# Kernel optimization log

Measured on AMD Instinct MI355X. Metric: run time of the kernel, lower is better.

## Reference

```python
import jax, jax.numpy as jnp
import numpy as np

B, N, DIM, H, DH = 8, 1024, 768, 12, 64
INNER = H * DH
SCALE = DH ** -0.5


def _bias_idx(n):
    # Reproduce the offset->id mapping from the torch __init__ loop:
    # offsets are first seen in row-major (p1, p2) order, so
    # id(0)=0, id(-k)=k (k=1..n-1), id(+k)=n-1+k.
    i = np.arange(n)[:, None]
    j = np.arange(n)[None, :]
    off = i - j
    idx = np.where(off <= 0, -off, n - 1 + off)
    return jnp.asarray(idx, dtype=jnp.int32)  # (n, n), values in [0, 2n-2]


def setup_inputs() -> dict:
    key = jax.random.key(0)
    ks = jax.random.split(key, 5)
    x = jax.random.normal(ks[0], (B, N, DIM), dtype=jnp.float32)
    w_qkv = jax.random.normal(ks[1], (DIM, 3 * INNER), dtype=jnp.float32) * (DIM ** -0.5)
    bias_table = jax.random.normal(ks[2], (H, 2 * N - 1), dtype=jnp.float32) * 0.02
    w_out = jax.random.normal(ks[3], (INNER, DIM), dtype=jnp.float32) * (INNER ** -0.5)
    b_out = jnp.zeros((DIM,), dtype=jnp.float32)
    bias_idx = _bias_idx(N)
    return {"x": x, "w_qkv": w_qkv, "bias_table": bias_table,
            "w_out": w_out, "b_out": b_out, "bias_idx": bias_idx}


def reference(x, w_qkv, bias_table, w_out, b_out, bias_idx):
    b, n, _ = x.shape
    qkv = x @ w_qkv  # (b, n, 3*inner)
    q, k, v = jnp.split(qkv, 3, axis=-1)
    def heads(t):
        return t.reshape(b, n, H, DH).transpose(0, 2, 1, 3)  # (b, h, n, d)
    q, k, v = heads(q), heads(k), heads(v)
    bias = bias_table[:, bias_idx]  # (h, n, n), gathered per-head relpos bias
    dots = jnp.einsum('bhid,bhjd->bhij', q, k) * SCALE + bias[None]
    attn = jax.nn.softmax(dots, axis=-1)
    out = jnp.einsum('bhij,bhjd->bhid', attn, v)
    out = out.transpose(0, 2, 1, 3).reshape(b, n, INNER)
    return out @ w_out + b_out
```

## Files before the change

### kernel.cpp

```cpp
#include <hip/hip_runtime.h>
#include <hip/hip_bf16.h>
#include <stdint.h>

typedef unsigned short u16;
typedef unsigned int u32;
typedef __bf16 bf16x8 __attribute__((ext_vector_type(8)));
typedef _Float16 f16x8 __attribute__((ext_vector_type(8)));
typedef float f32x4 __attribute__((ext_vector_type(4)));
typedef float f32x16 __attribute__((ext_vector_type(16)));
typedef unsigned short u16x4 __attribute__((ext_vector_type(4)));
typedef unsigned int u32x4 __attribute__((ext_vector_type(4)));

#define SEQ     1024
#define DIM     768
#define NH      12
#define QKV_LD  2304
#define LOG2E   1.4426950408889634f
#define C1      0.18033688f

__device__ __forceinline__ float bf2f(u16 u) {
    union { unsigned v; float f; } x; x.v = ((unsigned)u) << 16; return x.f;
}
__device__ __forceinline__ u16 f2bf(float f) {
    union { float f; unsigned v; } x; x.f = f;
    unsigned r = (x.v + 0x7FFFu + ((x.v >> 16) & 1u)) >> 16;
    return (u16)r;
}
__device__ __forceinline__ void store_out(u16* p, float v)  { *p = f2bf(v); }
__device__ __forceinline__ void store_out(float* p, float v){ *p = v; }

__device__ __forceinline__ void async16(void* lds, const void* g) {
    __builtin_amdgcn_global_load_lds(
        (const __attribute__((address_space(1))) unsigned*)(uintptr_t)g,
        (__attribute__((address_space(3))) unsigned*)(unsigned)(uintptr_t)lds,
        16, 0, 0);
}

__global__ __launch_bounds__(256) void cvt_k(const float* __restrict__ in,
                                             u16* __restrict__ out) {
    int i = (blockIdx.x * 256 + threadIdx.x) * 4;
    float4 v = *(const float4*)(in + i);
    u16x4 o = { f2bf(v.x), f2bf(v.y), f2bf(v.z), f2bf(v.w) };
    *(u16x4*)(out + i) = o;
}

__global__ __launch_bounds__(256) void transpose_k(const float* __restrict__ in,
                                                   u16* __restrict__ out,
                                                   int R, int C) {
    __shared__ __align__(16) float t[32][33];
    int c0 = blockIdx.x * 32, r0 = blockIdx.y * 32;
    int tx = threadIdx.x & 31, ty = threadIdx.x >> 5;
#pragma unroll
    for (int i = 0; i < 32; i += 8)
        t[ty + i][tx] = in[(size_t)(r0 + ty + i) * C + c0 + tx];
    __syncthreads();
#pragma unroll
    for (int i = 0; i < 32; i += 8)
        out[(size_t)(c0 + ty + i) * R + r0 + tx] = f2bf(t[tx][ty + i]);
}

__global__ __launch_bounds__(256) void vt_k(const u16* __restrict__ qkv,
                                            _Float16* __restrict__ vT) {
    __shared__ __align__(16) u16 t[32][33];
    int bh = blockIdx.z;
    int b = bh / 12, h = bh % 12;
    int key0 = blockIdx.x * 32, dh0 = blockIdx.y * 32;
    int tx = threadIdx.x & 31, ty = threadIdx.x >> 5;
#pragma unroll
    for (int i = 0; i < 32; i += 8)
        t[ty + i][tx] = qkv[(size_t)(b * SEQ + key0 + ty + i) * QKV_LD +
                            1536 + h * 64 + dh0 + tx];
    __syncthreads();
#pragma unroll
    for (int i = 0; i < 32; i += 8)
        vT[(size_t)(bh * 64 + dh0 + ty + i) * SEQ + key0 + tx] =
            (_Float16)bf2f(t[tx][ty + i]);
}

template <int HAS_BIAS, typename OUT_T>
__global__ __launch_bounds__(256) void gemm_bt(const u16* __restrict__ A,
                                               const u16* __restrict__ Bt,
                                               const float* __restrict__ bias,
                                               OUT_T* __restrict__ C,
                                               int M, int N, int K) {
    __shared__ __align__(16) u16 sA[128 * 64];
    __shared__ __align__(16) u16 sB[128 * 64];
    const int tid = threadIdx.x;
    const int lane = tid & 63;
    const int quad = lane >> 4, l16 = lane & 15;
    const int wave = tid >> 6;
    const int m0 = blockIdx.x * 128, n0 = blockIdx.y * 128;
    const int wm = (wave >> 1) * 64, wn = (wave & 1) * 64;

    const int co0 = (quad ^ (l16 & 7)) * 8;
    f32x4 acc[4][4] = {};

    for (int k0 = 0; k0 < K; k0 += 64) {
        __syncthreads();
#pragma unroll
        for (int rep = 0; rep < 4; ++rep) {
            int i = rep * 256 + tid;
            int row = i >> 3;
            int c = (i & 7) ^ (row & 7);
            async16(&sA[i * 8], A + (size_t)(m0 + row) * K + k0 + c * 8);
            async16(&sB[i * 8], Bt + (size_t)(n0 + row) * K + k0 + c * 8);
        }
        __syncthreads();

#pragma unroll
        for (int ks = 0; ks < 2; ++ks) {
            const int co = co0 ^ (ks * 32);
            bf16x8 af[4], bfr[4];
#pragma unroll
            for (int mi = 0; mi < 4; ++mi)
                af[mi] = *(const bf16x8*)&sA[(wm + mi * 16 + l16) * 64 + co];
#pragma unroll
            for (int nj = 0; nj < 4; ++nj)
                bfr[nj] = *(const bf16x8*)&sB[(wn + nj * 16 + l16) * 64 + co];
#pragma unroll
            for (int mi = 0; mi < 4; ++mi)
#pragma unroll
                for (int nj = 0; nj < 4; ++nj)
                    acc[mi][nj] = __builtin_amdgcn_mfma_f32_16x16x32_bf16(
                        af[mi], bfr[nj], acc[mi][nj], 0, 0, 0);
        }
    }

#pragma unroll
    for (int mi = 0; mi < 4; ++mi) {
#pragma unroll
        for (int nj = 0; nj < 4; ++nj) {
            int col = n0 + wn + nj * 16 + l16;
            float bv = HAS_BIAS ? bias[col] : 0.0f;
#pragma unroll
            for (int r = 0; r < 4; ++r) {
                int row = m0 + wm + mi * 16 + quad * 4 + r;
                store_out(&C[(size_t)row * N + col], acc[mi][nj][r] + bv);
            }
        }
    }
}

__global__ __launch_bounds__(256, 3) void attn_k(const u16* __restrict__ qkv,
                                                 const _Float16* __restrict__ vT,
                                                 const float* __restrict__ bias_table,
                                                 u16* __restrict__ out) {
    __shared__ __align__(16) u16 sK[2][64 * 64];
    __shared__ __align__(16) _Float16 sV[2][64 * 64];
    __shared__ __align__(16) float sLut[2048];

    const int tid = threadIdx.x;
    const int wave = tid >> 6, lane = tid & 63;
    const int l31 = lane & 31, hi = lane >> 5;
    const int bh = blockIdx.x;
    const int b = bh / NH, h = bh % NH;
    const int q0 = blockIdx.y * 128, wq = wave * 32;

    for (int i = tid; i < 2047; i += 256)
        sLut[i] = LOG2E * bias_table[h * 2047 + (i <= 1023 ? 1023 - i : i)];

    bf16x8 qf[4];
#pragma unroll
    for (int ks = 0; ks < 4; ++ks)
        qf[ks] = *(const bf16x8*)(qkv +
            (size_t)(b * SEQ + q0 + wq + l31) * QKV_LD + h * 64 + ks * 16 + hi * 8);

    const u16* kgp[2];
    const _Float16* vgp[2];
    int lds_i[2];
#pragma unroll
    for (int rep = 0; rep < 2; ++rep) {
        int i = rep * 256 + wave * 64 + lane;
        int row = i >> 3;
        int c = (i & 7) ^ (row & 7);
        kgp[rep] = qkv + (size_t)(b * SEQ + row) * QKV_LD + 768 + h * 64 + c * 8;
        vgp[rep] = vT + (size_t)(bh * 64 + row) * SEQ + c * 8;
        lds_i[rep] = i * 8;
    }

    const int ib0 = 1023 + q0 + wq + l31;
    const int hi4 = hi * 4;

#pragma unroll
    for (int rep = 0; rep < 2; ++rep) {
        async16(&sK[0][lds_i[rep]], kgp[rep]);
        async16(&sV[0][lds_i[rep]], vgp[rep]);
        kgp[rep] += (size_t)64 * QKV_LD;
        vgp[rep] += 64;
    }
    __syncthreads();

    f32x16 o[2] = {};
    f32x16 osum = {};
    const u32x4 onebits = { 0x3C003C00u, 0x3C003C00u, 0x3C003C00u, 0x3C003C00u };
    const f16x8 ones = __builtin_bit_cast(f16x8, onebits);

    for (int kt = 0; kt < SEQ / 64; ++kt) {
        const int cur = kt & 1;
        if (kt + 1 < SEQ / 64) {
            const int nxt = cur ^ 1;
#pragma unroll
            for (int rep = 0; rep < 2; ++rep) {
                async16(&sK[nxt][lds_i[rep]], kgp[rep]);
                async16(&sV[nxt][lds_i[rep]], vgp[rep]);
                kgp[rep] += (size_t)64 * QKV_LD;
                vgp[rep] += 64;
            }
        }
        const u16* sKc = sK[cur];
        const _Float16* sVc = sV[cur];

        f16x8 pfrag[4];
#pragma unroll
        for (int t = 0; t < 2; ++t) {
            const u16* kr = sKc + (t * 32 + l31) * 64;
            f32x16 s = {};
#pragma unroll
            for (int ks = 0; ks < 4; ++ks) {
                int slot = (2 * ks + hi) ^ (l31 & 7);
                bf16x8 af = *(const bf16x8*)(kr + slot * 8);
                s = __builtin_amdgcn_mfma_f32_32x32x16_bf16(af, qf[ks], s, 0, 0, 0);
            }
            const int ibt = ib0 - kt * 64 - t * 32 - hi4;
            u32 wlo[4], whi[4];
#pragma unroll
            for (int g = 0; g < 4; ++g) {
                const float* bw = &sLut[ibt - 8 * g];
                float p0 = __builtin_amdgcn_exp2f(s[4 * g + 0] * C1 + bw[0]);
                float p1 = __builtin_amdgcn_exp2f(s[4 * g + 1] * C1 + bw[-1]);
                float p2 = __builtin_amdgcn_exp2f(s[4 * g + 2] * C1 + bw[-2]);
                float p3 = __builtin_amdgcn_exp2f(s[4 * g + 3] * C1 + bw[-3]);
                wlo[g] = __builtin_bit_cast(u32, __builtin_amdgcn_cvt_pkrtz(p0, p1));
                whi[g] = __builtin_bit_cast(u32, __builtin_amdgcn_cvt_pkrtz(p2, p3));
            }
#pragma unroll
            for (int c = 0; c < 2; ++c) {
                auto rlo = __builtin_amdgcn_permlane32_swap(
                    wlo[2 * c], wlo[2 * c + 1], false, false);
                auto rhi = __builtin_amdgcn_permlane32_swap(
                    whi[2 * c], whi[2 * c + 1], false, false);
                u32x4 f = { rlo[0], rhi[0], rlo[1], rhi[1] };
                pfrag[t * 2 + c] = __builtin_bit_cast(f16x8, f);
            }
        }

#pragma unroll
        for (int kg = 0; kg < 4; ++kg)
            osum = __builtin_amdgcn_mfma_f32_32x32x16_f16(ones, pfrag[kg], osum, 0, 0, 0);
#pragma unroll
        for (int dt = 0; dt < 2; ++dt) {
            const _Float16* vr = sVc + (dt * 32 + l31) * 64;
#pragma unroll
            for (int kg = 0; kg < 4; ++kg) {
                int slot = (2 * kg + hi) ^ (l31 & 7);
                f16x8 vf = *(const f16x8*)(vr + slot * 8);
                o[dt] = __builtin_amdgcn_mfma_f32_32x32x16_f16(vf, pfrag[kg], o[dt], 0, 0, 0);
            }
        }
        __syncthreads();
    }

    float inv = __builtin_amdgcn_rcpf(osum[0]);
    size_t rowbase = (size_t)(b * SEQ + q0 + wq + l31) * DIM + h * 64 + hi4;
#pragma unroll
    for (int dt = 0; dt < 2; ++dt) {
#pragma unroll
        for (int g = 0; g < 4; ++g) {
            u16x4 pk = { f2bf(o[dt][4 * g + 0] * inv), f2bf(o[dt][4 * g + 1] * inv),
                         f2bf(o[dt][4 * g + 2] * inv), f2bf(o[dt][4 * g + 3] * inv) };
            *(u16x4*)&out[rowbase + dt * 32 + 8 * g] = pk;
        }
    }
}

extern "C" void kernel_launch(void* const* d_in, const int* in_sizes, int n_in,
                              void* d_out, int out_size, void* d_ws, size_t ws_size,
                              hipStream_t stream) {
    const float* x          = (const float*)d_in[0];
    const float* w_qkv      = (const float*)d_in[1];
    const float* bias_table = (const float*)d_in[2];
    const float* w_out      = (const float*)d_in[3];
    const float* b_out      = (const float*)d_in[4];
    float* out = (float*)d_out;

    char* ws = (char*)d_ws;
    u16* ws_qkv        = (u16*)(ws);
    u16* ws_attn       = (u16*)(ws + 37748736);
    u16* ws_xb         = (u16*)(ws + 50331648);
    u16* ws_wqkvT      = (u16*)(ws + 62914560);
    u16* ws_woutT      = (u16*)(ws + 66453504);
    _Float16* ws_vT    = (_Float16*)(ws + 67633152);

    cvt_k<<<8 * 1024 * 768 / 1024, 256, 0, stream>>>(x, ws_xb);
    transpose_k<<<dim3(2304 / 32, 768 / 32), 256, 0, stream>>>(w_qkv, ws_wqkvT, 768, 2304);
    transpose_k<<<dim3(768 / 32, 768 / 32), 256, 0, stream>>>(w_out, ws_woutT, 768, 768);

    gemm_bt<0, u16><<<dim3(8192 / 128, 2304 / 128), 256, 0, stream>>>(
        ws_xb, ws_wqkvT, nullptr, ws_qkv, 8192, 2304, 768);

    vt_k<<<dim3(SEQ / 32, 2, 8 * NH), 256, 0, stream>>>(ws_qkv, ws_vT);

    attn_k<<<dim3(8 * NH, SEQ / 128, 1), 256, 0, stream>>>(ws_qkv, ws_vT, bias_table, ws_attn);

    gemm_bt<1, float><<<dim3(8192 / 128, 768 / 128), 256, 0, stream>>>(
        ws_attn, ws_woutT, b_out, out, 8192, 768, 768);
}
```

Measured before the change: 198.6 us.

## Software-pipeline attention loop so PV of previous tile overlaps QK and exp

Restructures the flash-attention inner loop so the P·V and row-sum MFMAs for tile kt-1 are issued alongside the QK^T MFMAs for tile kt. The V fragments are held in registers across iterations, and the exp/pack of the current scores runs after those matrix ops. The intent is to let exp/VALU work overlap MFMA latency rather than serialize behind it. s_setprio raises wave priority around the MFMA block. The cost is more live registers (vf[8], pf, sAcc), which could reduce occupancy or cause spills.

```diff
diff --git a/kernel.cpp b/kernel.cpp
--- a/kernel.cpp
+++ b/kernel.cpp
@@ -180,6 +180,7 @@
 
     const int ib0 = 1023 + q0 + wq + l31;
     const int hi4 = hi * 4;
+    const int l7 = l31 & 7;
 
 #pragma unroll
     for (int rep = 0; rep < 2; ++rep) {
@@ -195,70 +196,112 @@
     const u32x4 onebits = { 0x3C003C00u, 0x3C003C00u, 0x3C003C00u, 0x3C003C00u };
     const f16x8 ones = __builtin_bit_cast(f16x8, onebits);
 
-    for (int kt = 0; kt < SEQ / 64; ++kt) {
+    f16x8 pf[4];
+    f16x8 vf[8];
+
+#define QK_TILE(sKc, kt, sAcc)                                                 \
+    _Pragma("unroll")                                                          \
+    for (int t = 0; t < 2; ++t) {                                              \
+        const u16* kr = (sKc) + (t * 32 + l31) * 64;                           \
+        f32x16 s = {};                                                         \
+        _Pragma("unroll")                                                      \
+        for (int ks = 0; ks < 4; ++ks) {                                       \
+            int slot = (2 * ks + hi) ^ l7;                                     \
+            bf16x8 af = *(const bf16x8*)(kr + slot * 8);                       \
+            s = __builtin_amdgcn_mfma_f32_32x32x16_bf16(af, qf[ks], s, 0, 0, 0); \
+        }                                                                      \
+        sAcc[t] = s;                                                           \
+    }
+
+#define PV_PREV()                                                              \
+    _Pragma("unroll")                                                          \
+    for (int kg = 0; kg < 4; ++kg)                                             \
+        osum = __builtin_amdgcn_mfma_f32_32x32x16_f16(ones, pf[kg], osum, 0, 0, 0); \
+    _Pragma("unroll")                                                          \
+    for (int dt = 0; dt < 2; ++dt)                                             \
+        _Pragma("unroll")                                                      \
+        for (int kg = 0; kg < 4; ++kg)                                         \
+            o[dt] = __builtin_amdgcn_mfma_f32_32x32x16_f16(                    \
+                vf[dt * 4 + kg], pf[kg], o[dt], 0, 0, 0);
+
+#define LOAD_V(sVc)                                                            \
+    _Pragma("unroll")                                                          \
+    for (int dt = 0; dt < 2; ++dt) {                                           \
+        const _Float16* vr = (sVc) + (dt * 32 + l31) * 64;                     \
+        _Pragma("unroll")                                                      \
+        for (int kg = 0; kg < 4; ++kg) {                                       \
+            int slot = (2 * kg + hi) ^ l7;                                     \
+            vf[dt * 4 + kg] = *(const f16x8*)(vr + slot * 8);                  \
+        }                                                                      \
+    }
+
+#define EXP_PACK(kt, sAcc)                                                     \
+    _Pragma("unroll")                                                          \
+    for (int t = 0; t < 2; ++t) {                                              \
+        const int ibt = ib0 - (kt) * 64 - t * 32 - hi4;                        \
+        u32 wlo[4], whi[4];                                                    \
+        _Pragma("unroll")                                                      \
+        for (int g = 0; g < 4; ++g) {                                          \
+            const float* bw = &sLut[ibt - 8 * g];                              \
+            float p0 = __builtin_amdgcn_exp2f(sAcc[t][4 * g + 0] * C1 + bw[0]);  \
+            float p1 = __builtin_amdgcn_exp2f(sAcc[t][4 * g + 1] * C1 + bw[-1]); \
+            float p2 = __builtin_amdgcn_exp2f(sAcc[t][4 * g + 2] * C1 + bw[-2]); \
+            float p3 = __builtin_amdgcn_exp2f(sAcc[t][4 * g + 3] * C1 + bw[-3]); \
+            wlo[g] = __builtin_bit_cast(u32, __builtin_amdgcn_cvt_pkrtz(p0, p1)); \
+            whi[g] = __builtin_bit_cast(u32, __builtin_amdgcn_cvt_pkrtz(p2, p3)); \
+        }                                                                      \
+        _Pragma("unroll")                                                      \
+        for (int c = 0; c < 2; ++c) {                                          \
+            auto rlo = __builtin_amdgcn_permlane32_swap(                       \
+                wlo[2 * c], wlo[2 * c + 1], false, false);                     \
+            auto rhi = __builtin_amdgcn_permlane32_swap(                       \
+                whi[2 * c], whi[2 * c + 1], false, false);                     \
+            u32x4 fw = { rlo[0], rhi[0], rlo[1], rhi[1] };                     \
+            pf[t * 2 + c] = __builtin_bit_cast(f16x8, fw);                     \
+        }                                                                      \
+    }
+
+#define PREFETCH(nxt)                                                          \
+    _Pragma("unroll")                                                          \
+    for (int rep = 0; rep < 2; ++rep) {                                        \
+        async16(&sK[nxt][lds_i[rep]], kgp[rep]);                               \
+        async16(&sV[nxt][lds_i[rep]], vgp[rep]);                               \
+        kgp[rep] += (size_t)64 * QKV_LD;                                       \
+        vgp[rep] += 64;                                                        \
+    }
+
+    {
+        PREFETCH(1)
+        f32x16 sAcc[2];
+        QK_TILE(sK[0], 0, sAcc)
+        LOAD_V(sV[0])
+        EXP_PACK(0, sAcc)
+        __syncthreads();
+    }
+
+    for (int kt = 1; kt < SEQ / 64; ++kt) {
         const int cur = kt & 1;
-        if (kt + 1 < SEQ / 64) {
-            const int nxt = cur ^ 1;
-#pragma unroll
-            for (int rep = 0; rep < 2; ++rep) {
-                async16(&sK[nxt][lds_i[rep]], kgp[rep]);
-                async16(&sV[nxt][lds_i[rep]], vgp[rep]);
-                kgp[rep] += (size_t)64 * QKV_LD;
-                vgp[rep] += 64;
-            }
-        }
+        if (kt + 1 < SEQ / 64) { PREFETCH(cur ^ 1) }
         const u16* sKc = sK[cur];
         const _Float16* sVc = sV[cur];
 
-        f16x8 pfrag[4];
-#pragma unroll
-        for (int t = 0; t < 2; ++t) {
-            const u16* kr = sKc + (t * 32 + l31) * 64;
-            f32x16 s = {};
-#pragma unroll
-            for (int ks = 0; ks < 4; ++ks) {
-                int slot = (2 * ks + hi) ^ (l31 & 7);
-                bf16x8 af = *(const bf16x8*)(kr + slot * 8);
-                s = __builtin_amdgcn_mfma_f32_32x32x16_bf16(af, qf[ks], s, 0, 0, 0);
-            }
-            const int ibt = ib0 - kt * 64 - t * 32 - hi4;
-            u32 wlo[4], whi[4];
-#pragma unroll
-            for (int g = 0; g < 4; ++g) {
-                const float* bw = &sLut[ibt - 8 * g];
-                float p0 = __builtin_amdgcn_exp2f(s[4 * g + 0] * C1 + bw[0]);
-                float p1 = __builtin_amdgcn_exp2f(s[4 * g + 1] * C1 + bw[-1]);
-                float p2 = __builtin_amdgcn_exp2f(s[4 * g + 2] * C1 + bw[-2]);
-                float p3 = __builtin_amdgcn_exp2f(s[4 * g + 3] * C1 + bw[-3]);
-                wlo[g] = __builtin_bit_cast(u32, __builtin_amdgcn_cvt_pkrtz(p0, p1));
-                whi[g] = __builtin_bit_cast(u32, __builtin_amdgcn_cvt_pkrtz(p2, p3));
-            }
-#pragma unroll
-            for (int c = 0; c < 2; ++c) {
-                auto rlo = __builtin_amdgcn_permlane32_swap(
-                    wlo[2 * c], wlo[2 * c + 1], false, false);
-                auto rhi = __builtin_amdgcn_permlane32_swap(
-                    whi[2 * c], whi[2 * c + 1], false, false);
-                u32x4 f = { rlo[0], rhi[0], rlo[1], rhi[1] };
-                pfrag[t * 2 + c] = __builtin_bit_cast(f16x8, f);
-            }
-        }
-
-#pragma unroll
-        for (int kg = 0; kg < 4; ++kg)
-            osum = __builtin_amdgcn_mfma_f32_32x32x16_f16(ones, pfrag[kg], osum, 0, 0, 0);
-#pragma unroll
-        for (int dt = 0; dt < 2; ++dt) {
-            const _Float16* vr = sVc + (dt * 32 + l31) * 64;
-#pragma unroll
-            for (int kg = 0; kg < 4; ++kg) {
-                int slot = (2 * kg + hi) ^ (l31 & 7);
-                f16x8 vf = *(const f16x8*)(vr + slot * 8);
-                o[dt] = __builtin_amdgcn_mfma_f32_32x32x16_f16(vf, pfrag[kg], o[dt], 0, 0, 0);
-            }
-        }
-        __syncthreads();
-    }
+        f32x16 sAcc[2];
+        __builtin_amdgcn_s_setprio(1);
+        QK_TILE(sKc, kt, sAcc)
+        PV_PREV()
+        __builtin_amdgcn_s_setprio(0);
+        LOAD_V(sVc)
+        EXP_PACK(kt, sAcc)
+        if (kt + 1 < SEQ / 64) __syncthreads();
+    }
+
+    PV_PREV()
+
+#undef QK_TILE
+#undef PV_PREV
+#undef LOAD_V
+#undef EXP_PACK
+#undef PREFETCH
 
     float inv = __builtin_amdgcn_rcpf(osum[0]);
     size_t rowbase = (size_t)(b * SEQ + q0 + wq + l31) * DIM + h * 64 + hi4;
```

Result: no change. 198.4 us (-0.1%).

## Load V fragments directly from global and use fp16 shifted bias LUTs

Applied to the files above, without the earlier changes.

The attention kernel no longer stages V tiles through shared memory. Each wave reads its V fragments straight from global memory into registers at the start of each key tile. The fp32 bias LUT is replaced by four pre-shifted fp16 copies, so each lane can fetch four consecutive bias values with one aligned vector load instead of four scalar loads. QK MFMAs are also grouped before the softmax, and the PV MFMAs run under raised wave priority. This cuts LDS usage, which may allow more occupancy, but it exposes global-load latency on V and adds fp16 rounding to the bias.

```diff
diff --git a/kernel.cpp b/kernel.cpp
--- a/kernel.cpp
+++ b/kernel.cpp
@@ -6,6 +6,7 @@
 typedef unsigned int u32;
 typedef __bf16 bf16x8 __attribute__((ext_vector_type(8)));
 typedef _Float16 f16x8 __attribute__((ext_vector_type(8)));
+typedef _Float16 f16x4 __attribute__((ext_vector_type(4)));
 typedef float f32x4 __attribute__((ext_vector_type(4)));
 typedef float f32x16 __attribute__((ext_vector_type(16)));
 typedef unsigned short u16x4 __attribute__((ext_vector_type(4)));
@@ -146,8 +147,7 @@
                                                  const float* __restrict__ bias_table,
                                                  u16* __restrict__ out) {
     __shared__ __align__(16) u16 sK[2][64 * 64];
-    __shared__ __align__(16) _Float16 sV[2][64 * 64];
-    __shared__ __align__(16) float sLut[2048];
+    __shared__ __align__(16) _Float16 sLutH[4 * 2052];
 
     const int tid = threadIdx.x;
     const int wave = tid >> 6, lane = tid & 63;
@@ -156,8 +156,15 @@
     const int b = bh / NH, h = bh % NH;
     const int q0 = blockIdx.y * 128, wq = wave * 32;
 
-    for (int i = tid; i < 2047; i += 256)
-        sLut[i] = LOG2E * bias_table[h * 2047 + (i <= 1023 ? 1023 - i : i)];
+#pragma unroll
+    for (int j = 0; j < 4; ++j)
+        for (int u = tid; u < 2052; u += 256) {
+            int z = 2047 - u - j;
+            float v = 0.f;
+            if (z >= 0 && z <= 2046)
+                v = LOG2E * bias_table[h * 2047 + (z <= 1023 ? 1023 - z : z)];
+            sLutH[j * 2052 + u] = (_Float16)v;
+        }
 
     bf16x8 qf[4];
 #pragma unroll
@@ -166,7 +173,6 @@
             (size_t)(b * SEQ + q0 + wq + l31) * QKV_LD + h * 64 + ks * 16 + hi * 8);
 
     const u16* kgp[2];
-    const _Float16* vgp[2];
     int lds_i[2];
 #pragma unroll
     for (int rep = 0; rep < 2; ++rep) {
@@ -174,19 +180,21 @@
         int row = i >> 3;
         int c = (i & 7) ^ (row & 7);
         kgp[rep] = qkv + (size_t)(b * SEQ + row) * QKV_LD + 768 + h * 64 + c * 8;
-        vgp[rep] = vT + (size_t)(bh * 64 + row) * SEQ + c * 8;
         lds_i[rep] = i * 8;
     }
 
-    const int ib0 = 1023 + q0 + wq + l31;
+    const _Float16* vb0 = vT + (size_t)(bh * 64 + l31) * SEQ + hi * 8;
+
+    const int r0 = (-l31) & 3;
+    const _Float16* lutp = sLutH + (r0 * 2052 - r0);
+    const int ub0 = 1024 - q0 - wq - l31 + hi * 4;
+    const int l7 = l31 & 7;
     const int hi4 = hi * 4;
 
 #pragma unroll
     for (int rep = 0; rep < 2; ++rep) {
         async16(&sK[0][lds_i[rep]], kgp[rep]);
-        async16(&sV[0][lds_i[rep]], vgp[rep]);
         kgp[rep] += (size_t)64 * QKV_LD;
-        vgp[rep] += 64;
     }
     __syncthreads();
 
@@ -198,38 +206,49 @@
     for (int kt = 0; kt < SEQ / 64; ++kt) {
         const int cur = kt & 1;
         if (kt + 1 < SEQ / 64) {
-            const int nxt = cur ^ 1;
 #pragma unroll
             for (int rep = 0; rep < 2; ++rep) {
-                async16(&sK[nxt][lds_i[rep]], kgp[rep]);
-                async16(&sV[nxt][lds_i[rep]], vgp[rep]);
+                async16(&sK[cur ^ 1][lds_i[rep]], kgp[rep]);
                 kgp[rep] += (size_t)64 * QKV_LD;
-                vgp[rep] += 64;
-            }
-        }
+            }
+        }
+
+        f16x8 vf[8];
+#pragma unroll
+        for (int dt = 0; dt < 2; ++dt)
+#pragma unroll
+            for (int kg = 0; kg < 4; ++kg)
+                vf[dt * 4 + kg] =
+                    *(const f16x8*)(vb0 + (size_t)dt * 32 * SEQ + kt * 64 + kg * 16);
+
         const u16* sKc = sK[cur];
-        const _Float16* sVc = sV[cur];
-
-        f16x8 pfrag[4];
+
+        f32x16 sAcc[2];
 #pragma unroll
         for (int t = 0; t < 2; ++t) {
             const u16* kr = sKc + (t * 32 + l31) * 64;
             f32x16 s = {};
 #pragma unroll
             for (int ks = 0; ks < 4; ++ks) {
-                int slot = (2 * ks + hi) ^ (l31 & 7);
+                int slot = (2 * ks + hi) ^ l7;
                 bf16x8 af = *(const bf16x8*)(kr + slot * 8);
                 s = __builtin_amdgcn_mfma_f32_32x32x16_bf16(af, qf[ks], s, 0, 0, 0);
             }
-            const int ibt = ib0 - kt * 64 - t * 32 - hi4;
+            sAcc[t] = s;
+        }
+
+        f16x8 pf[4];
+#pragma unroll
+        for (int t = 0; t < 2; ++t) {
+            const int ub = ub0 + kt * 64 + t * 32;
             u32 wlo[4], whi[4];
 #pragma unroll
             for (int g = 0; g < 4; ++g) {
-                const float* bw = &sLut[ibt - 8 * g];
-                float p0 = __builtin_amdgcn_exp2f(s[4 * g + 0] * C1 + bw[0]);
-                float p1 = __builtin_amdgcn_exp2f(s[4 * g + 1] * C1 + bw[-1]);
-                float p2 = __builtin_amdgcn_exp2f(s[4 * g + 2] * C1 + bw[-2]);
-                float p3 = __builtin_amdgcn_exp2f(s[4 * g + 3] * C1 + bw[-3]);
+                f16x4 bw4 = *(const f16x4*)(lutp + ub + 8 * g);
+                float p0 = __builtin_amdgcn_exp2f(sAcc[t][4 * g + 0] * C1 + (float)bw4[0]);
+                float p1 = __builtin_amdgcn_exp2f(sAcc[t][4 * g + 1] * C1 + (float)bw4[1]);
+                float p2 = __builtin_amdgcn_exp2f(sAcc[t][4 * g + 2] * C1 + (float)bw4[2]);
+                float p3 = __builtin_amdgcn_exp2f(sAcc[t][4 * g + 3] * C1 + (float)bw4[3]);
                 wlo[g] = __builtin_bit_cast(u32, __builtin_amdgcn_cvt_pkrtz(p0, p1));
                 whi[g] = __builtin_bit_cast(u32, __builtin_amdgcn_cvt_pkrtz(p2, p3));
             }
@@ -239,24 +258,23 @@
                     wlo[2 * c], wlo[2 * c + 1], false, false);
                 auto rhi = __builtin_amdgcn_permlane32_swap(
                     whi[2 * c], whi[2 * c + 1], false, false);
-                u32x4 f = { rlo[0], rhi[0], rlo[1], rhi[1] };
-                pfrag[t * 2 + c] = __builtin_bit_cast(f16x8, f);
-            }
-        }
-
+                u32x4 fw = { rlo[0], rhi[0], rlo[1], rhi[1] };
+                pf[t * 2 + c] = __builtin_bit_cast(f16x8, fw);
+            }
+        }
+
+        __builtin_amdgcn_s_setprio(1);
 #pragma unroll
         for (int kg = 0; kg < 4; ++kg)
-            osum = __builtin_amdgcn_mfma_f32_32x32x16_f16(ones, pfrag[kg], osum, 0, 0, 0);
-#pragma unroll
-        for (int dt = 0; dt < 2; ++dt) {
-            const _Float16* vr = sVc + (dt * 32 + l31) * 64;
-#pragma unroll
-            for (int kg = 0; kg < 4; ++kg) {
-                int slot = (2 * kg + hi) ^ (l31 & 7);
-                f16x8 vf = *(const f16x8*)(vr + slot * 8);
-                o[dt] = __builtin_amdgcn_mfma_f32_32x32x16_f16(vf, pfrag[kg], o[dt], 0, 0, 0);
-            }
-        }
+            osum = __builtin_amdgcn_mfma_f32_32x32x16_f16(ones, pf[kg], osum, 0, 0, 0);
+#pragma unroll
+        for (int dt = 0; dt < 2; ++dt)
+#pragma unroll
+            for (int kg = 0; kg < 4; ++kg)
+                o[dt] = __builtin_amdgcn_mfma_f32_32x32x16_f16(
+                    vf[dt * 4 + kg], pf[kg], o[dt], 0, 0, 0);
+        __builtin_amdgcn_s_setprio(0);
+
         __syncthreads();
     }
 
```

New measurement: 215.6 us. 1.09x slower.

## Pre-swizzle K and V into MFMA fragment layout and drop LDS staging in attention

Applied to the files above, without the earlier changes.

Adds prep kernels that rewrite K and V per head into the exact per-lane MFMA fragment order, so the attention kernel loads operands straight from global memory into registers. This removes the LDS double buffer, async copies and per-tile barriers, and the kernel now raises wave priority around the PV MFMAs. The GEMM also remaps workgroup IDs so that each XCD works on a contiguous range of M tiles, aiming at better L2 reuse. The cost is one extra prep launch plus more global and L2 traffic per wave, since every wave reloads K and V without sharing them through LDS. ws_xb is reused as the K-fragment buffer once the QKV GEMM has finished with it.

```diff
diff --git a/kernel.cpp b/kernel.cpp
--- a/kernel.cpp
+++ b/kernel.cpp
@@ -9,6 +9,7 @@
 typedef float f32x4 __attribute__((ext_vector_type(4)));
 typedef float f32x16 __attribute__((ext_vector_type(16)));
 typedef unsigned short u16x4 __attribute__((ext_vector_type(4)));
+typedef unsigned short u16x8 __attribute__((ext_vector_type(8)));
 typedef unsigned int u32x4 __attribute__((ext_vector_type(4)));
 
 #define SEQ     1024
@@ -59,22 +60,52 @@
         out[(size_t)(c0 + ty + i) * R + r0 + tx] = f2bf(t[tx][ty + i]);
 }
 
-__global__ __launch_bounds__(256) void vt_k(const u16* __restrict__ qkv,
-                                            _Float16* __restrict__ vT) {
-    __shared__ __align__(16) u16 t[32][33];
-    int bh = blockIdx.z;
-    int b = bh / 12, h = bh % 12;
-    int key0 = blockIdx.x * 32, dh0 = blockIdx.y * 32;
-    int tx = threadIdx.x & 31, ty = threadIdx.x >> 5;
-#pragma unroll
-    for (int i = 0; i < 32; i += 8)
-        t[ty + i][tx] = qkv[(size_t)(b * SEQ + key0 + ty + i) * QKV_LD +
-                            1536 + h * 64 + dh0 + tx];
+__global__ __launch_bounds__(256) void kprep_k(const u16* __restrict__ qkv,
+                                               u16* __restrict__ kf) {
+    __shared__ u16 t2[64][68];
+    const int kt = blockIdx.x, bh = blockIdx.y;
+    const int b = bh / NH, h = bh % NH;
+    const int tid = threadIdx.x;
+    const int row = tid >> 2, c0 = (tid & 3) * 16;
+    const u16* src = qkv + (size_t)(b * SEQ + kt * 64 + row) * QKV_LD + 768 + h * 64 + c0;
+#pragma unroll
+    for (int q = 0; q < 4; ++q)
+        *(u16x4*)&t2[row][c0 + q * 4] = *(const u16x4*)(src + q * 4);
     __syncthreads();
 #pragma unroll
-    for (int i = 0; i < 32; i += 8)
-        vT[(size_t)(bh * 64 + dh0 + ty + i) * SEQ + key0 + tx] =
-            (_Float16)bf2f(t[tx][ty + i]);
+    for (int u = tid; u < 512; u += 256) {
+        int f = u >> 6, lane = u & 63;
+        int t = f >> 2, ks = f & 3;
+        int hi = lane >> 5, l31 = lane & 31;
+        const u16* p = &t2[t * 32 + l31][ks * 16 + hi * 8];
+        u16x8 w = { p[0], p[1], p[2], p[3], p[4], p[5], p[6], p[7] };
+        *(u16x8*)&kf[((((size_t)bh * 16 + kt) * 8 + f) * 64 + lane) * 8] = w;
+    }
+}
+
+__global__ __launch_bounds__(256) void vprep_k(const u16* __restrict__ qkv,
+                                               _Float16* __restrict__ vf) {
+    __shared__ u16 t2[64][68];
+    const int kt = blockIdx.x, bh = blockIdx.y;
+    const int b = bh / NH, h = bh % NH;
+    const int tid = threadIdx.x;
+    const int row = tid >> 2, c0 = (tid & 3) * 16;
+    const u16* src = qkv + (size_t)(b * SEQ + kt * 64 + row) * QKV_LD + 1536 + h * 64 + c0;
+#pragma unroll
+    for (int q = 0; q < 4; ++q)
+        *(u16x4*)&t2[row][c0 + q * 4] = *(const u16x4*)(src + q * 4);
+    __syncthreads();
+#pragma unroll
+    for (int u = tid; u < 512; u += 256) {
+        int c = u >> 6, lane = u & 63;
+        int dt = c >> 2, kg = c & 3;
+        int hi = lane >> 5, l31 = lane & 31;
+        f16x8 w;
+#pragma unroll
+        for (int j = 0; j < 8; ++j)
+            w[j] = (_Float16)bf2f(t2[kg * 16 + hi * 8 + j][dt * 32 + l31]);
+        *(f16x8*)&vf[((((size_t)bh * 16 + kt) * 8 + c) * 64 + lane) * 8] = w;
+    }
 }
 
 template <int HAS_BIAS, typename OUT_T>
@@ -89,7 +120,12 @@
     const int lane = tid & 63;
     const int quad = lane >> 4, l16 = lane & 15;
     const int wave = tid >> 6;
-    const int m0 = blockIdx.x * 128, n0 = blockIdx.y * 128;
+
+    const int wgid = blockIdx.y * gridDim.x + blockIdx.x;
+    const int xcd = wgid & 7, idx = wgid >> 3;
+    const int CM = gridDim.x >> 3;
+    const int m0 = (xcd * CM + idx % CM) * 128;
+    const int n0 = (idx / CM) * 128;
     const int wm = (wave >> 1) * 64, wn = (wave & 1) * 64;
 
     const int co0 = (quad ^ (l16 & 7)) * 8;
@@ -142,11 +178,10 @@
 }
 
 __global__ __launch_bounds__(256, 3) void attn_k(const u16* __restrict__ qkv,
-                                                 const _Float16* __restrict__ vT,
+                                                 const u16* __restrict__ kfr,
+                                                 const _Float16* __restrict__ vfr,
                                                  const float* __restrict__ bias_table,
                                                  u16* __restrict__ out) {
-    __shared__ __align__(16) u16 sK[2][64 * 64];
-    __shared__ __align__(16) _Float16 sV[2][64 * 64];
     __shared__ __align__(16) float sLut[2048];
 
     const int tid = threadIdx.x;
@@ -165,29 +200,12 @@
         qf[ks] = *(const bf16x8*)(qkv +
             (size_t)(b * SEQ + q0 + wq + l31) * QKV_LD + h * 64 + ks * 16 + hi * 8);
 
-    const u16* kgp[2];
-    const _Float16* vgp[2];
-    int lds_i[2];
-#pragma unroll
-    for (int rep = 0; rep < 2; ++rep) {
-        int i = rep * 256 + wave * 64 + lane;
-        int row = i >> 3;
-        int c = (i & 7) ^ (row & 7);
-        kgp[rep] = qkv + (size_t)(b * SEQ + row) * QKV_LD + 768 + h * 64 + c * 8;
-        vgp[rep] = vT + (size_t)(bh * 64 + row) * SEQ + c * 8;
-        lds_i[rep] = i * 8;
-    }
+    const u16* kp = kfr + ((size_t)bh * 16 * 8 * 64 + lane) * 8;
+    const _Float16* vp = vfr + ((size_t)bh * 16 * 8 * 64 + lane) * 8;
 
     const int ib0 = 1023 + q0 + wq + l31;
     const int hi4 = hi * 4;
 
-#pragma unroll
-    for (int rep = 0; rep < 2; ++rep) {
-        async16(&sK[0][lds_i[rep]], kgp[rep]);
-        async16(&sV[0][lds_i[rep]], vgp[rep]);
-        kgp[rep] += (size_t)64 * QKV_LD;
-        vgp[rep] += 64;
-    }
     __syncthreads();
 
     f32x16 o[2] = {};
@@ -196,31 +214,22 @@
     const f16x8 ones = __builtin_bit_cast(f16x8, onebits);
 
     for (int kt = 0; kt < SEQ / 64; ++kt) {
-        const int cur = kt & 1;
-        if (kt + 1 < SEQ / 64) {
-            const int nxt = cur ^ 1;
-#pragma unroll
-            for (int rep = 0; rep < 2; ++rep) {
-                async16(&sK[nxt][lds_i[rep]], kgp[rep]);
-                async16(&sV[nxt][lds_i[rep]], vgp[rep]);
-                kgp[rep] += (size_t)64 * QKV_LD;
-                vgp[rep] += 64;
-            }
-        }
-        const u16* sKc = sK[cur];
-        const _Float16* sVc = sV[cur];
+        f16x8 vf[8];
+#pragma unroll
+        for (int c = 0; c < 8; ++c)
+            vf[c] = *(const f16x8*)(vp + (size_t)(kt * 8 + c) * 512);
 
         f16x8 pfrag[4];
 #pragma unroll
         for (int t = 0; t < 2; ++t) {
-            const u16* kr = sKc + (t * 32 + l31) * 64;
+            bf16x8 kf4[4];
+#pragma unroll
+            for (int ks = 0; ks < 4; ++ks)
+                kf4[ks] = *(const bf16x8*)(kp + (size_t)(kt * 8 + t * 4 + ks) * 512);
             f32x16 s = {};
 #pragma unroll
-            for (int ks = 0; ks < 4; ++ks) {
-                int slot = (2 * ks + hi) ^ (l31 & 7);
-                bf16x8 af = *(const bf16x8*)(kr + slot * 8);
-                s = __builtin_amdgcn_mfma_f32_32x32x16_bf16(af, qf[ks], s, 0, 0, 0);
-            }
+            for (int ks = 0; ks < 4; ++ks)
+                s = __builtin_amdgcn_mfma_f32_32x32x16_bf16(kf4[ks], qf[ks], s, 0, 0, 0);
             const int ibt = ib0 - kt * 64 - t * 32 - hi4;
             u32 wlo[4], whi[4];
 #pragma unroll
@@ -244,20 +253,17 @@
             }
         }
 
+        __builtin_amdgcn_s_setprio(1);
 #pragma unroll
         for (int kg = 0; kg < 4; ++kg)
             osum = __builtin_amdgcn_mfma_f32_32x32x16_f16(ones, pfrag[kg], osum, 0, 0, 0);
 #pragma unroll
-        for (int dt = 0; dt < 2; ++dt) {
-            const _Float16* vr = sVc + (dt * 32 + l31) * 64;
-#pragma unroll
-            for (int kg = 0; kg < 4; ++kg) {
-                int slot = (2 * kg + hi) ^ (l31 & 7);
-                f16x8 vf = *(const f16x8*)(vr + slot * 8);
-                o[dt] = __builtin_amdgcn_mfma_f32_32x32x16_f16(vf, pfrag[kg], o[dt], 0, 0, 0);
-            }
-        }
-        __syncthreads();
+        for (int dt = 0; dt < 2; ++dt)
+#pragma unroll
+            for (int kg = 0; kg < 4; ++kg)
+                o[dt] = __builtin_amdgcn_mfma_f32_32x32x16_f16(
+                    vf[dt * 4 + kg], pfrag[kg], o[dt], 0, 0, 0);
+        __builtin_amdgcn_s_setprio(0);
     }
 
     float inv = __builtin_amdgcn_rcpf(osum[0]);
@@ -298,9 +304,11 @@
     gemm_bt<0, u16><<<dim3(8192 / 128, 2304 / 128), 256, 0, stream>>>(
         ws_xb, ws_wqkvT, nullptr, ws_qkv, 8192, 2304, 768);
 
-    vt_k<<<dim3(SEQ / 32, 2, 8 * NH), 256, 0, stream>>>(ws_qkv, ws_vT);
-
-    attn_k<<<dim3(8 * NH, SEQ / 128, 1), 256, 0, stream>>>(ws_qkv, ws_vT, bias_table, ws_attn);
+    kprep_k<<<dim3(16, 96), 256, 0, stream>>>(ws_qkv, ws_xb);
+    vprep_k<<<dim3(16, 96), 256, 0, stream>>>(ws_qkv, ws_vT);
+
+    attn_k<<<dim3(8 * NH, SEQ / 128, 1), 256, 0, stream>>>(
+        ws_qkv, ws_xb, ws_vT, bias_table, ws_attn);
 
     gemm_bt<1, float><<<dim3(8192 / 128, 768 / 128), 256, 0, stream>>>(
         ws_attn, ws_woutT, b_out, out, 8192, 768, 768);
```

After: 209.4 us. +5.5%, slower.
